# Kernel tuning notes

Measured on AMD Instinct MI355X. Metric: run time of the kernel, lower is better.

Reference implementation:

```python
import jax, jax.numpy as jnp
import numpy as np

H = 16   # num_heads
K = 2    # top_k experts per token


def _layer_norm(x, g, b, eps=1e-5):
    mu = jnp.mean(x, axis=-1, keepdims=True)
    var = jnp.mean(jnp.square(x - mu), axis=-1, keepdims=True)
    return (x - mu) * jax.lax.rsqrt(var + eps) * g + b


def setup_inputs() -> dict:
    key = jax.random.key(0)
    ks = jax.random.split(key, 8)
    B, S, D, E = 2, 2048, 1024, 8
    sc = 0.02
    return {
        "x": jax.random.normal(ks[0], (B, S, D), jnp.float32),
        "wq": jax.random.normal(ks[1], (D, D), jnp.float32) * sc,
        "wk": jax.random.normal(ks[2], (D, D), jnp.float32) * sc,
        "wv": jax.random.normal(ks[3], (D, D), jnp.float32) * sc,
        "wo": jax.random.normal(ks[4], (D, D), jnp.float32) * sc,
        "ln1_g": jnp.ones((D,), jnp.float32),
        "ln1_b": jnp.zeros((D,), jnp.float32),
        "ln2_g": jnp.ones((D,), jnp.float32),
        "ln2_b": jnp.zeros((D,), jnp.float32),
        "router_w": jax.random.normal(ks[5], (E, D), jnp.float32) * sc,
        "expert_w": jax.random.normal(ks[6], (E, D, D), jnp.float32) * sc,
    }


def reference(x, wq, wk, wv, wo, ln1_g, ln1_b, ln2_g, ln2_b, router_w, expert_w):
    B, S, D = x.shape
    E = expert_w.shape[0]
    hd = D // H

    # ---- attention sublayer: x = x + attn(norm1(x)) ----
    h = _layer_norm(x, ln1_g, ln1_b)
    q = (h @ wq.T).reshape(B, S, H, hd).transpose(0, 2, 1, 3)  # bhsd
    k = (h @ wk.T).reshape(B, S, H, hd).transpose(0, 2, 1, 3)
    v = (h @ wv.T).reshape(B, S, H, hd).transpose(0, 2, 1, 3)
    scores = jnp.einsum("bhqd,bhkd->bhqk", q, k) / jnp.sqrt(jnp.float32(hd))
    causal = jnp.tril(jnp.ones((S, S), dtype=bool))
    scores = jnp.where(causal, scores, jnp.finfo(scores.dtype).min)
    probs = jax.nn.softmax(scores, axis=-1)
    attn = jnp.einsum("bhqk,bhkd->bhqd", probs, v)
    attn = attn.transpose(0, 2, 1, 3).reshape(B, S, D) @ wo.T
    x = x + attn

    # ---- MoE sublayer: x = x + moe(norm2(x)) ----
    h2 = _layer_norm(x, ln2_g, ln2_b)
    logits = jnp.einsum("bsd,ed->bse", h2, router_w)          # [B,S,E]
    top_logits, top_ids = jax.lax.top_k(logits, K)            # [B,S,K]
    gates = jax.nn.softmax(top_logits, axis=-1)               # [B,S,K]
    # dense combine weights over experts (E is small): sum_k gate_k * onehot(id_k)
    combine = jnp.sum(jax.nn.one_hot(top_ids, E, dtype=h2.dtype) * gates[..., None], axis=-2)  # [B,S,E]
    # per-token matvec with expert weights: token @ W_e.T for each expert, then weighted sum
    y = jnp.einsum("bsd,eod->bseo", h2, expert_w)             # [B,S,E,D]
    moe_out = jnp.einsum("bse,bseo->bso", combine, y)
    return x + moe_out
```

## Files before the change

kernel.cpp:

```cpp
#include <hip/hip_runtime.h>
#include <hip/hip_bf16.h>
#include <cstdint>


typedef __bf16 bf16;
typedef __bf16 bf16x8 __attribute__((ext_vector_type(8)));
typedef __bf16 bf16x4 __attribute__((ext_vector_type(4)));
typedef float f32x4 __attribute__((ext_vector_type(4)));
typedef float f32x16 __attribute__((ext_vector_type(16)));

#define MFMA(a, b, c) __builtin_amdgcn_mfma_f32_16x16x32_bf16(a, b, c, 0, 0, 0)
#define MFMA32(a, b, c) __builtin_amdgcn_mfma_f32_32x32x16_bf16(a, b, c, 0, 0, 0)

__device__ __forceinline__ void gld16(void* lds, const void* g) {
  __builtin_amdgcn_global_load_lds(
      (const __attribute__((address_space(1))) void*)g,
      (__attribute__((address_space(3))) void*)lds, 16, 0, 0);
}

__device__ __forceinline__ uint32_t pack_hilo(float pv) {
  bf16 h = (bf16)pv;
  bf16 l = (bf16)(pv - (float)h);
  union { bf16 b[2]; uint32_t u; } cv;
  cv.b[0] = h; cv.b[1] = l;
  return cv.u;
}

__global__ void prep_weights(const float* __restrict__ wq, const float* __restrict__ wk,
                             const float* __restrict__ wv, const float* __restrict__ wo,
                             const float* __restrict__ expw,
                             bf16* __restrict__ wqh, bf16* __restrict__ wql,
                             bf16* __restrict__ wkh, bf16* __restrict__ wkl,
                             bf16* __restrict__ wvh, bf16* __restrict__ wvl,
                             bf16* __restrict__ woh, bf16* __restrict__ wol,
                             bf16* __restrict__ ewh) {
  int bid = blockIdx.x;
  if (bid < 4096) {
    int wsel = bid >> 10;
    const float* src = wsel == 0 ? wq : wsel == 1 ? wk : wsel == 2 ? wv : wo;
    bf16* hi = wsel == 0 ? wqh : wsel == 1 ? wkh : wsel == 2 ? wvh : woh;
    bf16* lo = wsel == 0 ? wql : wsel == 1 ? wkl : wsel == 2 ? wvl : wol;
    int i = ((bid & 1023) * 256 + threadIdx.x) * 4;
    float4 v = *(const float4*)(src + i);
    float a[4] = {v.x, v.y, v.z, v.w};
#pragma unroll
    for (int j = 0; j < 4; j++) {
      bf16 h = (bf16)a[j];
      hi[i + j] = h;
      lo[i + j] = (bf16)(a[j] - (float)h);
    }
  } else {
    int i = ((bid - 4096) * 256 + threadIdx.x) * 4;
    float4 v = *(const float4*)(expw + i);
    ewh[i] = (bf16)v.x; ewh[i + 1] = (bf16)v.y;
    ewh[i + 2] = (bf16)v.z; ewh[i + 3] = (bf16)v.w;
  }
}

__global__ void ln_split(const float* __restrict__ x, const float* __restrict__ g,
                         const float* __restrict__ b, bf16* __restrict__ hi,
                         bf16* __restrict__ lo) {
  int tok = blockIdx.x, t = threadIdx.x;
  float4 v = ((const float4*)(x + (size_t)tok * 1024))[t];
  float s = v.x + v.y + v.z + v.w;
  float ss = v.x * v.x + v.y * v.y + v.z * v.z + v.w * v.w;
#pragma unroll
  for (int o = 1; o < 64; o <<= 1) { s += __shfl_xor(s, o); ss += __shfl_xor(ss, o); }
  __shared__ float red[8];
  int w = t >> 6, lane = t & 63;
  if (lane == 0) { red[w] = s; red[4 + w] = ss; }
  __syncthreads();
  s = red[0] + red[1] + red[2] + red[3];
  ss = red[4] + red[5] + red[6] + red[7];
  float mu = s * (1.f / 1024.f);
  float rstd = rsqrtf(ss * (1.f / 1024.f) - mu * mu + 1e-5f);
  float4 gv = ((const float4*)g)[t], bv = ((const float4*)b)[t];
  float y[4] = {(v.x - mu) * rstd * gv.x + bv.x, (v.y - mu) * rstd * gv.y + bv.y,
                (v.z - mu) * rstd * gv.z + bv.z, (v.w - mu) * rstd * gv.w + bv.w};
  size_t o = (size_t)tok * 1024 + t * 4;
#pragma unroll
  for (int j = 0; j < 4; j++) {
    bf16 h = (bf16)y[j];
    hi[o + j] = h;
    lo[o + j] = (bf16)(y[j] - (float)h);
  }
}

__global__ void ln2route(const float* __restrict__ x1, const float* __restrict__ g,
                         const float* __restrict__ b, const float* __restrict__ rw,
                         bf16* __restrict__ h2h, int* __restrict__ eid,
                         float2* __restrict__ gout) {
  int tok = blockIdx.x, t = threadIdx.x;
  float4 v = ((const float4*)(x1 + (size_t)tok * 1024))[t];
  float s = v.x + v.y + v.z + v.w;
  float ss = v.x * v.x + v.y * v.y + v.z * v.z + v.w * v.w;
#pragma unroll
  for (int o = 1; o < 64; o <<= 1) { s += __shfl_xor(s, o); ss += __shfl_xor(ss, o); }
  __shared__ float red[8];
  __shared__ float h2s[1024];
  __shared__ float lg[8];
  int w = t >> 6, lane = t & 63;
  if (lane == 0) { red[w] = s; red[4 + w] = ss; }
  __syncthreads();
  s = red[0] + red[1] + red[2] + red[3];
  ss = red[4] + red[5] + red[6] + red[7];
  float mu = s * (1.f / 1024.f);
  float rstd = rsqrtf(ss * (1.f / 1024.f) - mu * mu + 1e-5f);
  float4 gv = ((const float4*)g)[t], bv = ((const float4*)b)[t];
  float4 y;
  y.x = (v.x - mu) * rstd * gv.x + bv.x;
  y.y = (v.y - mu) * rstd * gv.y + bv.y;
  y.z = (v.z - mu) * rstd * gv.z + bv.z;
  y.w = (v.w - mu) * rstd * gv.w + bv.w;
  ((float4*)h2s)[t] = y;
  size_t o = (size_t)tok * 1024 + t * 4;
  h2h[o] = (bf16)y.x; h2h[o + 1] = (bf16)y.y;
  h2h[o + 2] = (bf16)y.z; h2h[o + 3] = (bf16)y.w;
  __syncthreads();
  float a0 = 0.f, a1 = 0.f;
  const float4* r0 = (const float4*)(rw + (2 * w) * 1024);
  const float4* r1 = (const float4*)(rw + (2 * w + 1) * 1024);
#pragma unroll
  for (int it = 0; it < 4; it++) {
    float4 xv = ((const float4*)h2s)[lane + 64 * it];
    float4 w0 = r0[lane + 64 * it];
    float4 w1 = r1[lane + 64 * it];
    a0 += xv.x * w0.x + xv.y * w0.y + xv.z * w0.z + xv.w * w0.w;
    a1 += xv.x * w1.x + xv.y * w1.y + xv.z * w1.z + xv.w * w1.w;
  }
#pragma unroll
  for (int o2 = 1; o2 < 64; o2 <<= 1) {
    a0 += __shfl_xor(a0, o2);
    a1 += __shfl_xor(a1, o2);
  }
  if (lane == 0) { lg[2 * w] = a0; lg[2 * w + 1] = a1; }
  __syncthreads();
  if (t == 0) {
    int i0 = 0; float l0 = lg[0];
#pragma unroll
    for (int e = 1; e < 8; e++) if (lg[e] > l0) { l0 = lg[e]; i0 = e; }
    int i1 = -1; float l1 = -3e38f;
#pragma unroll
    for (int e = 0; e < 8; e++) if (e != i0 && lg[e] > l1) { l1 = lg[e]; i1 = e; }
    float e1 = __expf(l1 - l0);
    float den = 1.f + e1;
    eid[tok] = i0 | (i1 << 4);
    gout[tok] = make_float2(1.f / den, e1 / den);
  }
}

__global__ void build_lists(const int* __restrict__ eid,
                            const float2* __restrict__ gv,
                            int* __restrict__ tlist, float* __restrict__ glist,
                            int* __restrict__ cnt) {
  int e = blockIdx.x, t = threadIdx.x;
  int lane = t & 63, w = t >> 6;
  __shared__ int wt[4];
  int base = 0;
  for (int c = 0; c < 16; c++) {
    int tok = c * 256 + t;
    int pair = eid[tok];
    int e0 = pair & 15, e1 = pair >> 4;
    bool p = (e0 == e) || (e1 == e);
    float2 g2 = gv[tok];
    float gate = (e0 == e) ? g2.x : g2.y;
    unsigned long long m = __ballot(p);
    int rank = __popcll(m & ((1ull << lane) - 1ull));
    if (lane == 0) wt[w] = __popcll(m);
    __syncthreads();
    int off = base;
    for (int i = 0; i < w; i++) off += wt[i];
    if (p) {
      tlist[e * 4096 + off + rank] = tok;
      glist[e * 4096 + off + rank] = gate;
    }
    base += wt[0] + wt[1] + wt[2] + wt[3];
    __syncthreads();
  }
  if (t == 0) cnt[e] = base;
  int pad = (base + 127) & ~127;
  if (pad > 4096) pad = 4096;
  for (int i = base + t; i < pad; i += 256) {
    tlist[e * 4096 + i] = 0;
    glist[e * 4096 + i] = 0.f;
  }
}

__device__ __forceinline__ void gemm_core_split(
    const bf16* __restrict__ Ah, const bf16* __restrict__ Al,
    const bf16* __restrict__ Bh, const bf16* __restrict__ Bl, int m0, int n0,
    f32x4 (&acc)[4][4]) {
  __shared__ __align__(16) bf16 As_h[4096], As_l[4096], Bs_h[4096], Bs_l[4096];
  int t = threadIdx.x, lane = t & 63, w = t >> 6;
  int i0 = t, i1 = t + 256;
  const bf16* a0h = Ah + (size_t)(m0 + (i0 >> 2)) * 1024 + (i0 & 3) * 8;
  const bf16* a1h = Ah + (size_t)(m0 + (i1 >> 2)) * 1024 + (i1 & 3) * 8;
  const bf16* a0l = Al + (size_t)(m0 + (i0 >> 2)) * 1024 + (i0 & 3) * 8;
  const bf16* a1l = Al + (size_t)(m0 + (i1 >> 2)) * 1024 + (i1 & 3) * 8;
  const bf16* b0h = Bh + (size_t)(n0 + (i0 >> 2)) * 1024 + (i0 & 3) * 8;
  const bf16* b1h = Bh + (size_t)(n0 + (i1 >> 2)) * 1024 + (i1 & 3) * 8;
  const bf16* b0l = Bl + (size_t)(n0 + (i0 >> 2)) * 1024 + (i0 & 3) * 8;
  const bf16* b1l = Bl + (size_t)(n0 + (i1 >> 2)) * 1024 + (i1 & 3) * 8;
  int wm = (w >> 1) * 64, wn = (w & 1) * 64;
  int lr = lane & 15, lq = lane >> 4;
  for (int k0 = 0; k0 < 1024; k0 += 32) {
    __syncthreads();
    gld16(&As_h[i0 * 8], a0h + k0); gld16(&As_h[i1 * 8], a1h + k0);
    gld16(&As_l[i0 * 8], a0l + k0); gld16(&As_l[i1 * 8], a1l + k0);
    gld16(&Bs_h[i0 * 8], b0h + k0); gld16(&Bs_h[i1 * 8], b1h + k0);
    gld16(&Bs_l[i0 * 8], b0l + k0); gld16(&Bs_l[i1 * 8], b1l + k0);
    __syncthreads();
    bf16x8 ah[4], al4[4], bh[4], bl4[4];
#pragma unroll
    for (int i = 0; i < 4; i++) {
      ah[i]  = *(const bf16x8*)&As_h[(wm + i * 16 + lr) * 32 + lq * 8];
      al4[i] = *(const bf16x8*)&As_l[(wm + i * 16 + lr) * 32 + lq * 8];
      bh[i]  = *(const bf16x8*)&Bs_h[(wn + i * 16 + lr) * 32 + lq * 8];
      bl4[i] = *(const bf16x8*)&Bs_l[(wn + i * 16 + lr) * 32 + lq * 8];
    }
#pragma unroll
    for (int i = 0; i < 4; i++)
#pragma unroll
      for (int j = 0; j < 4; j++) {
        f32x4 c = acc[i][j];
        c = MFMA(ah[i], bh[j], c);
        c = MFMA(ah[i], bl4[j], c);
        c = MFMA(al4[i], bh[j], c);
        acc[i][j] = c;
      }
  }
}

__global__ __launch_bounds__(256, 2) void gemm_qkv(
    const bf16* __restrict__ hh, const bf16* __restrict__ hl,
    const bf16* __restrict__ wqh, const bf16* __restrict__ wql,
    const bf16* __restrict__ wkh, const bf16* __restrict__ wkl,
    const bf16* __restrict__ wvh, const bf16* __restrict__ wvl,
    bf16* __restrict__ qh, bf16* __restrict__ ql, bf16* __restrict__ kh,
    bf16* __restrict__ kl, bf16* __restrict__ vth, bf16* __restrict__ vtl) {
  int n0 = blockIdx.x * 128, m0 = blockIdx.y * 128, z = blockIdx.z;
  const bf16 *Bh = wqh, *Bl = wql;
  if (z == 1) { Bh = wkh; Bl = wkl; }
  if (z == 2) { Bh = wvh; Bl = wvl; }
  f32x4 acc[4][4];
#pragma unroll
  for (int i = 0; i < 4; i++)
#pragma unroll
    for (int j = 0; j < 4; j++) acc[i][j] = (f32x4){0.f, 0.f, 0.f, 0.f};
  gemm_core_split(hh, hl, Bh, Bl, m0, n0, acc);
  int t = threadIdx.x, lane = t & 63, w = t >> 6;
  int wm = (w >> 1) * 64, wn = (w & 1) * 64, lr = lane & 15, lq = lane >> 4;
  if (z < 2) {
    bf16* Oh = z == 0 ? qh : kh;
    bf16* Ol = z == 0 ? ql : kl;
    float scale = (z == 0) ? (0.125f * 1.44269504f) : 1.0f;
#pragma unroll
    for (int i = 0; i < 4; i++)
#pragma unroll
      for (int j = 0; j < 4; j++)
#pragma unroll
        for (int r = 0; r < 4; r++) {
          size_t row = m0 + wm + i * 16 + lq * 4 + r;
          int col = n0 + wn + j * 16 + lr;
          float v = acc[i][j][r] * scale;
          bf16 h = (bf16)v;
          Oh[row * 1024 + col] = h;
          Ol[row * 1024 + col] = (bf16)(v - (float)h);
        }
  } else {
    int bb = m0 >> 11;
    int srow0 = m0 & 2047;
#pragma unroll
    for (int i = 0; i < 4; i++)
#pragma unroll
      for (int j = 0; j < 4; j++) {
        int col = n0 + wn + j * 16 + lr;
        int head = col >> 6, d = col & 63;
        int s = srow0 + wm + i * 16 + lq * 4;
        bf16x4 hv, lv;
#pragma unroll
        for (int r = 0; r < 4; r++) {
          float v = acc[i][j][r];
          bf16 h = (bf16)v;
          hv[r] = h;
          lv[r] = (bf16)(v - (float)h);
        }
        size_t off = ((size_t)((bb * 16 + head) * 64 + d)) * 2048 + s;
        *(bf16x4*)(vth + off) = hv;
        *(bf16x4*)(vtl + off) = lv;
      }
  }
}

__global__ __launch_bounds__(256, 2) void gemm_wo(
    const bf16* __restrict__ ah, const bf16* __restrict__ al,
    const bf16* __restrict__ bh, const bf16* __restrict__ bl,
    const float* __restrict__ resid, float* __restrict__ outp) {
  int n0 = blockIdx.x * 128, m0 = blockIdx.y * 128;
  f32x4 acc[4][4];
#pragma unroll
  for (int i = 0; i < 4; i++)
#pragma unroll
    for (int j = 0; j < 4; j++) acc[i][j] = (f32x4){0.f, 0.f, 0.f, 0.f};
  gemm_core_split(ah, al, bh, bl, m0, n0, acc);
  int t = threadIdx.x, lane = t & 63, w = t >> 6;
  int wm = (w >> 1) * 64, wn = (w & 1) * 64, lr = lane & 15, lq = lane >> 4;
#pragma unroll
  for (int i = 0; i < 4; i++)
#pragma unroll
    for (int j = 0; j < 4; j++)
#pragma unroll
      for (int r = 0; r < 4; r++) {
        size_t row = m0 + wm + i * 16 + lq * 4 + r;
        int col = n0 + wn + j * 16 + lr;
        outp[row * 1024 + col] = resid[row * 1024 + col] + acc[i][j][r];
      }
}

__global__ __launch_bounds__(256, 2) void attn_fused(
    const bf16* __restrict__ qh, const bf16* __restrict__ ql,
    const bf16* __restrict__ kh, const bf16* __restrict__ kl,
    const bf16* __restrict__ vth, const bf16* __restrict__ vtl,
    bf16* __restrict__ oh, bf16* __restrict__ ol) {
  const int S = 2048, D = 1024;
  int qt = 15 - blockIdx.y;
  int hb = blockIdx.x;
  int head = hb & 15, b = hb >> 4;
  int qb = qt * 128;
  int t = threadIdx.x, lane = t & 63, w = t >> 6;
  int l31 = lane & 31, l5 = lane >> 5;
  int base = b * S, hcol = head * 64;

  __shared__ __align__(16) bf16 Kh_s[4096], Kl_s[4096];
  __shared__ __align__(16) bf16 Vh_s[4096], Vl_s[4096];
  __shared__ __align__(16) uint32_t Pp[4][32 * 68];

  bf16x8 qfh[4], qfl[4];
  {
    const bf16* p1 = qh + (size_t)(base + qb + w * 32 + l31) * D + hcol + l5 * 8;
    const bf16* p2 = ql + (size_t)(base + qb + w * 32 + l31) * D + hcol + l5 * 8;
#pragma unroll
    for (int c = 0; c < 4; c++) {
      qfh[c] = *(const bf16x8*)(p1 + 16 * c);
      qfl[c] = *(const bf16x8*)(p2 + 16 * c);
    }
  }
  f32x16 O0, O1;
  float lrow[16];
#pragma unroll
  for (int r = 0; r < 16; r++) { O0[r] = 0.f; O1[r] = 0.f; lrow[r] = 0.f; }

  int r0 = t >> 3, p0 = t & 7;
  int r1 = 32 + r0;
  int g0 = p0 ^ (r0 & 7);
  const bf16* k0hp = kh + (size_t)(base + r0) * D + hcol + g0 * 8;
  const bf16* k1hp = kh + (size_t)(base + r1) * D + hcol + g0 * 8;
  const bf16* k0lp = kl + (size_t)(base + r0) * D + hcol + g0 * 8;
  const bf16* k1lp = kl + (size_t)(base + r1) * D + hcol + g0 * 8;
  const bf16* v0hp = vth + (size_t)(hb * 64 + r0) * 2048 + g0 * 8;
  const bf16* v1hp = vth + (size_t)(hb * 64 + r1) * 2048 + g0 * 8;
  const bf16* v0lp = vtl + (size_t)(hb * 64 + r0) * 2048 + g0 * 8;
  const bf16* v1lp = vtl + (size_t)(hb * 64 + r1) * 2048 + g0 * 8;

  int qwmin = qb + w * 32;

  for (int kt = 0; kt <= qb + 64; kt += 64) {
    __syncthreads();
    gld16(&Kh_s[t * 8], k0hp + (size_t)kt * D);
    gld16(&Kh_s[2048 + t * 8], k1hp + (size_t)kt * D);
    gld16(&Kl_s[t * 8], k0lp + (size_t)kt * D);
    gld16(&Kl_s[2048 + t * 8], k1lp + (size_t)kt * D);
    gld16(&Vh_s[t * 8], v0hp + kt);
    gld16(&Vh_s[2048 + t * 8], v1hp + kt);
    gld16(&Vl_s[t * 8], v0lp + kt);
    gld16(&Vl_s[2048 + t * 8], v1lp + kt);
    __syncthreads();
    if (kt > qwmin + 31) continue;
    bool mask0 = (kt + 31 > qwmin);
    bool skip1 = (kt + 32 > qwmin + 31);
    bool mask1 = (kt + 63 > qwmin);
#pragma unroll
    for (int ktile = 0; ktile < 2; ktile++) {
      if (ktile == 1 && skip1) break;
      int keyr = ktile * 32 + l31;
      f32x16 sc;
#pragma unroll
      for (int r = 0; r < 16; r++) sc[r] = 0.f;
#pragma unroll
      for (int c = 0; c < 4; c++) {
        int dg = ((2 * c + l5) ^ (keyr & 7)) * 8;
        bf16x8 kv = *(const bf16x8*)&Kh_s[keyr * 64 + dg];
        bf16x8 km = *(const bf16x8*)&Kl_s[keyr * 64 + dg];
        sc = MFMA32(qfh[c], kv, sc);
        sc = MFMA32(qfl[c], kv, sc);
        sc = MFMA32(qfh[c], km, sc);
      }
      bool m = ktile ? mask1 : mask0;
      int keyg = kt + keyr;
      uint32_t* prow = &Pp[w][ktile * 32 + l31];
#pragma unroll
      for (int r = 0; r < 16; r++) {
        int qlocal = (r & 3) + 8 * (r >> 2) + 4 * l5;
        float sv = sc[r];
        if (m && keyg > qwmin + qlocal) sv = -30000.f;
        float pv = __builtin_amdgcn_exp2f(sv);
        lrow[r] += pv;
        prow[qlocal * 68] = pack_hilo(pv);
      }
    }
#pragma unroll
    for (int c = 0; c < 4; c++) {
      if (skip1 && c >= 2) break;
      const uint32_t* pr = &Pp[w][l31 * 68 + 16 * c + l5 * 8];
      uint32_t pd[8];
      *(uint4*)&pd[0] = *(const uint4*)&pr[0];
      *(uint4*)&pd[4] = *(const uint4*)&pr[4];
      union { uint32_t u[4]; bf16x8 v; } ph_, pl_;
#pragma unroll
      for (int i = 0; i < 4; i++) {
        ph_.u[i] = __builtin_amdgcn_perm(pd[2 * i + 1], pd[2 * i], 0x05040100u);
        pl_.u[i] = __builtin_amdgcn_perm(pd[2 * i + 1], pd[2 * i], 0x07060302u);
      }
#pragma unroll
      for (int dtile = 0; dtile < 2; dtile++) {
        int d = dtile * 32 + l31;
        int kg = ((2 * c + l5) ^ (d & 7)) * 8;
        bf16x8 vb = *(const bf16x8*)&Vh_s[d * 64 + kg];
        bf16x8 vm = *(const bf16x8*)&Vl_s[d * 64 + kg];
        if (dtile == 0) {
          O0 = MFMA32(ph_.v, vb, O0);
          O0 = MFMA32(pl_.v, vb, O0);
          O0 = MFMA32(ph_.v, vm, O0);
        } else {
          O1 = MFMA32(ph_.v, vb, O1);
          O1 = MFMA32(pl_.v, vb, O1);
          O1 = MFMA32(ph_.v, vm, O1);
        }
      }
    }
  }
#pragma unroll
  for (int r = 0; r < 16; r++) {
    float l = lrow[r];
    l += __shfl_xor(l, 1); l += __shfl_xor(l, 2); l += __shfl_xor(l, 4);
    l += __shfl_xor(l, 8); l += __shfl_xor(l, 16);
    float linv = 1.f / l;
    int qlocal = (r & 3) + 8 * (r >> 2) + 4 * l5;
    size_t tok = (size_t)(base + qb + w * 32 + qlocal);
    float v0 = O0[r] * linv;
    float v1 = O1[r] * linv;
    bf16 h0 = (bf16)v0, h1 = (bf16)v1;
    oh[tok * D + hcol + l31] = h0;
    ol[tok * D + hcol + l31] = (bf16)(v0 - (float)h0);
    oh[tok * D + hcol + 32 + l31] = h1;
    ol[tok * D + hcol + 32 + l31] = (bf16)(v1 - (float)h1);
  }
}

__global__ __launch_bounds__(256, 2) void gemm_moe(
    const bf16* __restrict__ A, const bf16* __restrict__ W,
    const int* __restrict__ tlist, const float* __restrict__ glist,
    const int* __restrict__ cnt, float* __restrict__ outp) {
  int e = blockIdx.z;
  int count = cnt[e];
  int m0 = blockIdx.y * 128;
  if (m0 >= count) return;
  int n0 = blockIdx.x * 128;
  const int* tl = tlist + e * 4096;
  const bf16* B = W + (size_t)e * 1024 * 1024;
  __shared__ __align__(16) bf16 As[4096], Bs[4096];
  int t = threadIdx.x, lane = t & 63, w = t >> 6;
  int i0 = t, i1 = t + 256;
  int ra = tl[m0 + (i0 >> 2)], rb = tl[m0 + (i1 >> 2)];
  const bf16* a0 = A + (size_t)ra * 1024 + (i0 & 3) * 8;
  const bf16* a1 = A + (size_t)rb * 1024 + (i1 & 3) * 8;
  const bf16* b0 = B + (size_t)(n0 + (i0 >> 2)) * 1024 + (i0 & 3) * 8;
  const bf16* b1 = B + (size_t)(n0 + (i1 >> 2)) * 1024 + (i1 & 3) * 8;
  int wm = (w >> 1) * 64, wn = (w & 1) * 64, lr = lane & 15, lq = lane >> 4;
  f32x4 acc[4][4];
#pragma unroll
  for (int i = 0; i < 4; i++)
#pragma unroll
    for (int j = 0; j < 4; j++) acc[i][j] = (f32x4){0.f, 0.f, 0.f, 0.f};
  for (int k0 = 0; k0 < 1024; k0 += 32) {
    __syncthreads();
    gld16(&As[i0 * 8], a0 + k0); gld16(&As[i1 * 8], a1 + k0);
    gld16(&Bs[i0 * 8], b0 + k0); gld16(&Bs[i1 * 8], b1 + k0);
    __syncthreads();
    bf16x8 af[4], bfr[4];
#pragma unroll
    for (int i = 0; i < 4; i++) {
      af[i] = *(const bf16x8*)&As[(wm + i * 16 + lr) * 32 + lq * 8];
      bfr[i] = *(const bf16x8*)&Bs[(wn + i * 16 + lr) * 32 + lq * 8];
    }
#pragma unroll
    for (int i = 0; i < 4; i++)
#pragma unroll
      for (int j = 0; j < 4; j++) acc[i][j] = MFMA(af[i], bfr[j], acc[i][j]);
  }
#pragma unroll
  for (int i = 0; i < 4; i++)
#pragma unroll
    for (int r = 0; r < 4; r++) {
      int slot = m0 + wm + i * 16 + lq * 4 + r;
      if (slot < count) {
        int tok = tl[slot];
        float gte = glist[e * 4096 + slot];
#pragma unroll
        for (int j = 0; j < 4; j++) {
          int col = n0 + wn + j * 16 + lr;
          atomicAdd(&outp[(size_t)tok * 1024 + col], gte * acc[i][j][r]);
        }
      }
    }
}

extern "C" void kernel_launch(void* const* d_in, const int* in_sizes, int n_in,
                              void* d_out, int out_size, void* d_ws, size_t ws_size,
                              hipStream_t stream) {
  (void)in_sizes; (void)n_in; (void)out_size; (void)ws_size;
  const float* x    = (const float*)d_in[0];
  const float* wq   = (const float*)d_in[1];
  const float* wk   = (const float*)d_in[2];
  const float* wv   = (const float*)d_in[3];
  const float* wo   = (const float*)d_in[4];
  const float* ln1g = (const float*)d_in[5];
  const float* ln1b = (const float*)d_in[6];
  const float* ln2g = (const float*)d_in[7];
  const float* ln2b = (const float*)d_in[8];
  const float* rw   = (const float*)d_in[9];
  const float* expw = (const float*)d_in[10];
  float* out = (float*)d_out;

  char* p = (char*)d_ws;
  auto take = [&](size_t bytes) -> char* {
    char* r = p;
    p += (bytes + 255) & ~(size_t)255;
    return r;
  };
  const size_t ND2 = 4096ull * 1024 * 2;
  const size_t WD2 = 1024ull * 1024 * 2;
  bf16* h_hi = (bf16*)take(ND2); bf16* h_lo = (bf16*)take(ND2);
  bf16* wqh = (bf16*)take(WD2); bf16* wql = (bf16*)take(WD2);
  bf16* wkh = (bf16*)take(WD2); bf16* wkl = (bf16*)take(WD2);
  bf16* wvh = (bf16*)take(WD2); bf16* wvl = (bf16*)take(WD2);
  bf16* woh = (bf16*)take(WD2); bf16* wol = (bf16*)take(WD2);
  bf16* q_hi = (bf16*)take(ND2); bf16* q_lo = (bf16*)take(ND2);
  bf16* k_hi = (bf16*)take(ND2); bf16* k_lo = (bf16*)take(ND2);
  bf16* vt_hi = (bf16*)take(ND2); bf16* vt_lo = (bf16*)take(ND2);
  bf16* a_hi = (bf16*)take(ND2); bf16* a_lo = (bf16*)take(ND2);
  bf16* h2h  = (bf16*)take(ND2);
  bf16* ewh  = (bf16*)take(8ull * 1024 * 1024 * 2);
  int*   tlist  = (int*)take(8ull * 4096 * 4);
  float* glist  = (float*)take(8ull * 4096 * 4);
  int*   cnt    = (int*)take(64);
  int*   reid   = (int*)take(4096 * 4);
  float2* rg    = (float2*)take(4096 * 8);

  prep_weights<<<12288, 256, 0, stream>>>(wq, wk, wv, wo, expw, wqh, wql, wkh,
                                          wkl, wvh, wvl, woh, wol, ewh);
  ln_split<<<4096, 256, 0, stream>>>(x, ln1g, ln1b, h_hi, h_lo);
  gemm_qkv<<<dim3(8, 32, 3), 256, 0, stream>>>(h_hi, h_lo, wqh, wql, wkh, wkl,
                                               wvh, wvl, q_hi, q_lo, k_hi, k_lo,
                                               vt_hi, vt_lo);
  attn_fused<<<dim3(32, 16), 256, 0, stream>>>(q_hi, q_lo, k_hi, k_lo, vt_hi,
                                               vt_lo, a_hi, a_lo);
  gemm_wo<<<dim3(8, 32), 256, 0, stream>>>(a_hi, a_lo, woh, wol, x, out);
  ln2route<<<4096, 256, 0, stream>>>(out, ln2g, ln2b, rw, h2h, reid, rg);
  build_lists<<<8, 256, 0, stream>>>(reid, rg, tlist, glist, cnt);
  gemm_moe<<<dim3(8, 32, 8), 256, 0, stream>>>(h2h, ewh, tlist, glist, cnt,
                                               out);
}
```

Baseline: 414.6 us.

## Double-buffer attention K/V tiles in 32-key chunks and raise occupancy bounds

The attention kernel now streams K/V in 32-key chunks with two LDS buffers, prefetching the next chunk while computing the current one, and drops one of the two barriers per iteration. The V tile uses a new swizzle and the P scratch shrinks, which lowers LDS use. Q-tile scheduling is reordered so long and short causal tiles alternate. Launch bounds rise to 3 blocks per CU for attention and 4 for the GEMMs, which may force register spilling.

Result: slower. 442.2 us (+6.7%).

```diff
diff --git a/kernel.cpp b/kernel.cpp
--- a/kernel.cpp
+++ b/kernel.cpp
@@ -231,7 +231,7 @@
   }
 }
 
-__global__ __launch_bounds__(256, 2) void gemm_qkv(
+__global__ __launch_bounds__(256, 4) void gemm_qkv(
     const bf16* __restrict__ hh, const bf16* __restrict__ hl,
     const bf16* __restrict__ wqh, const bf16* __restrict__ wql,
     const bf16* __restrict__ wkh, const bf16* __restrict__ wkl,
@@ -292,7 +292,7 @@
   }
 }
 
-__global__ __launch_bounds__(256, 2) void gemm_wo(
+__global__ __launch_bounds__(256, 4) void gemm_wo(
     const bf16* __restrict__ ah, const bf16* __restrict__ al,
     const bf16* __restrict__ bh, const bf16* __restrict__ bl,
     const float* __restrict__ resid, float* __restrict__ outp) {
@@ -317,13 +317,14 @@
       }
 }
 
-__global__ __launch_bounds__(256, 2) void attn_fused(
+__global__ __launch_bounds__(256, 3) void attn_fused(
     const bf16* __restrict__ qh, const bf16* __restrict__ ql,
     const bf16* __restrict__ kh, const bf16* __restrict__ kl,
     const bf16* __restrict__ vth, const bf16* __restrict__ vtl,
     bf16* __restrict__ oh, bf16* __restrict__ ol) {
   const int S = 2048, D = 1024;
-  int qt = 15 - blockIdx.y;
+  int y = blockIdx.y;
+  int qt = (y < 8) ? (15 - y) : (y - 8);
   int hb = blockIdx.x;
   int head = hb & 15, b = hb >> 4;
   int qb = qt * 128;
@@ -331,9 +332,9 @@
   int l31 = lane & 31, l5 = lane >> 5;
   int base = b * S, hcol = head * 64;
 
-  __shared__ __align__(16) bf16 Kh_s[4096], Kl_s[4096];
-  __shared__ __align__(16) bf16 Vh_s[4096], Vl_s[4096];
-  __shared__ __align__(16) uint32_t Pp[4][32 * 68];
+  __shared__ __align__(16) bf16 Kh_s[2][2048], Kl_s[2][2048];
+  __shared__ __align__(16) bf16 Vh_s[2][2048], Vl_s[2][2048];
+  __shared__ __align__(16) uint32_t Pp[4][32 * 36];
 
   bf16x8 qfh[4], qfl[4];
   {
@@ -350,94 +351,92 @@
 #pragma unroll
   for (int r = 0; r < 16; r++) { O0[r] = 0.f; O1[r] = 0.f; lrow[r] = 0.f; }
 
-  int r0 = t >> 3, p0 = t & 7;
-  int r1 = 32 + r0;
-  int g0 = p0 ^ (r0 & 7);
-  const bf16* k0hp = kh + (size_t)(base + r0) * D + hcol + g0 * 8;
-  const bf16* k1hp = kh + (size_t)(base + r1) * D + hcol + g0 * 8;
-  const bf16* k0lp = kl + (size_t)(base + r0) * D + hcol + g0 * 8;
-  const bf16* k1lp = kl + (size_t)(base + r1) * D + hcol + g0 * 8;
-  const bf16* v0hp = vth + (size_t)(hb * 64 + r0) * 2048 + g0 * 8;
-  const bf16* v1hp = vth + (size_t)(hb * 64 + r1) * 2048 + g0 * 8;
-  const bf16* v0lp = vtl + (size_t)(hb * 64 + r0) * 2048 + g0 * 8;
-  const bf16* v1lp = vtl + (size_t)(hb * 64 + r1) * 2048 + g0 * 8;
+  int krow = t >> 3;
+  int kg = (t & 7) ^ (krow & 7);
+  const bf16* kph = kh + (size_t)(base + krow) * D + hcol + kg * 8;
+  const bf16* kpl = kl + (size_t)(base + krow) * D + hcol + kg * 8;
+  int vd = ((t >> 3) << 1) | ((t >> 2) & 1);
+  int vg = ((t & 3) - (t >> 3)) & 3;
+  const bf16* vph = vth + (size_t)(hb * 64 + vd) * 2048 + vg * 8;
+  const bf16* vpl = vtl + (size_t)(hb * 64 + vd) * 2048 + vg * 8;
 
   int qwmin = qb + w * 32;
-
-  for (int kt = 0; kt <= qb + 64; kt += 64) {
-    __syncthreads();
-    gld16(&Kh_s[t * 8], k0hp + (size_t)kt * D);
-    gld16(&Kh_s[2048 + t * 8], k1hp + (size_t)kt * D);
-    gld16(&Kl_s[t * 8], k0lp + (size_t)kt * D);
-    gld16(&Kl_s[2048 + t * 8], k1lp + (size_t)kt * D);
-    gld16(&Vh_s[t * 8], v0hp + kt);
-    gld16(&Vh_s[2048 + t * 8], v1hp + kt);
-    gld16(&Vl_s[t * 8], v0lp + kt);
-    gld16(&Vl_s[2048 + t * 8], v1lp + kt);
-    __syncthreads();
-    if (kt > qwmin + 31) continue;
-    bool mask0 = (kt + 31 > qwmin);
-    bool skip1 = (kt + 32 > qwmin + 31);
-    bool mask1 = (kt + 63 > qwmin);
-#pragma unroll
-    for (int ktile = 0; ktile < 2; ktile++) {
-      if (ktile == 1 && skip1) break;
-      int keyr = ktile * 32 + l31;
+  int nch = (qb + 128) >> 5;
+
+  gld16(&Kh_s[0][t * 8], kph);
+  gld16(&Kl_s[0][t * 8], kpl);
+  gld16(&Vh_s[0][t * 8], vph);
+  gld16(&Vl_s[0][t * 8], vpl);
+  __syncthreads();
+
+  for (int it = 0; it < nch; it++) {
+    int ib = it & 1;
+    if (it + 1 < nch) {
+      int jb = ib ^ 1;
+      size_t ko = (size_t)(it + 1) * 32 * D;
+      int vo = (it + 1) * 32;
+      gld16(&Kh_s[jb][t * 8], kph + ko);
+      gld16(&Kl_s[jb][t * 8], kpl + ko);
+      gld16(&Vh_s[jb][t * 8], vph + vo);
+      gld16(&Vl_s[jb][t * 8], vpl + vo);
+    }
+    int kt = it << 5;
+    if (kt <= qwmin + 31) {
+      bool need_mask = (kt + 31 > qwmin);
       f32x16 sc;
 #pragma unroll
       for (int r = 0; r < 16; r++) sc[r] = 0.f;
 #pragma unroll
       for (int c = 0; c < 4; c++) {
-        int dg = ((2 * c + l5) ^ (keyr & 7)) * 8;
-        bf16x8 kv = *(const bf16x8*)&Kh_s[keyr * 64 + dg];
-        bf16x8 km = *(const bf16x8*)&Kl_s[keyr * 64 + dg];
+        int pg = ((2 * c + l5) ^ (l31 & 7)) * 8;
+        bf16x8 kv = *(const bf16x8*)&Kh_s[ib][l31 * 64 + pg];
+        bf16x8 km = *(const bf16x8*)&Kl_s[ib][l31 * 64 + pg];
         sc = MFMA32(qfh[c], kv, sc);
         sc = MFMA32(qfl[c], kv, sc);
         sc = MFMA32(qfh[c], km, sc);
       }
-      bool m = ktile ? mask1 : mask0;
-      int keyg = kt + keyr;
-      uint32_t* prow = &Pp[w][ktile * 32 + l31];
+      uint32_t* prow = &Pp[w][l31];
 #pragma unroll
       for (int r = 0; r < 16; r++) {
         int qlocal = (r & 3) + 8 * (r >> 2) + 4 * l5;
         float sv = sc[r];
-        if (m && keyg > qwmin + qlocal) sv = -30000.f;
+        if (need_mask && kt + l31 > qwmin + qlocal) sv = -30000.f;
         float pv = __builtin_amdgcn_exp2f(sv);
         lrow[r] += pv;
-        prow[qlocal * 68] = pack_hilo(pv);
-      }
-    }
-#pragma unroll
-    for (int c = 0; c < 4; c++) {
-      if (skip1 && c >= 2) break;
-      const uint32_t* pr = &Pp[w][l31 * 68 + 16 * c + l5 * 8];
-      uint32_t pd[8];
-      *(uint4*)&pd[0] = *(const uint4*)&pr[0];
-      *(uint4*)&pd[4] = *(const uint4*)&pr[4];
-      union { uint32_t u[4]; bf16x8 v; } ph_, pl_;
-#pragma unroll
-      for (int i = 0; i < 4; i++) {
-        ph_.u[i] = __builtin_amdgcn_perm(pd[2 * i + 1], pd[2 * i], 0x05040100u);
-        pl_.u[i] = __builtin_amdgcn_perm(pd[2 * i + 1], pd[2 * i], 0x07060302u);
-      }
-#pragma unroll
-      for (int dtile = 0; dtile < 2; dtile++) {
-        int d = dtile * 32 + l31;
-        int kg = ((2 * c + l5) ^ (d & 7)) * 8;
-        bf16x8 vb = *(const bf16x8*)&Vh_s[d * 64 + kg];
-        bf16x8 vm = *(const bf16x8*)&Vl_s[d * 64 + kg];
-        if (dtile == 0) {
-          O0 = MFMA32(ph_.v, vb, O0);
-          O0 = MFMA32(pl_.v, vb, O0);
-          O0 = MFMA32(ph_.v, vm, O0);
-        } else {
-          O1 = MFMA32(ph_.v, vb, O1);
-          O1 = MFMA32(pl_.v, vb, O1);
-          O1 = MFMA32(ph_.v, vm, O1);
+        prow[qlocal * 36] = pack_hilo(pv);
+      }
+#pragma unroll
+      for (int kc = 0; kc < 2; kc++) {
+        const uint32_t* pr = &Pp[w][l31 * 36 + kc * 16 + l5 * 8];
+        uint32_t pd[8];
+        *(uint4*)&pd[0] = *(const uint4*)&pr[0];
+        *(uint4*)&pd[4] = *(const uint4*)&pr[4];
+        union { uint32_t u[4]; bf16x8 v; } ph_, pl_;
+#pragma unroll
+        for (int i = 0; i < 4; i++) {
+          ph_.u[i] = __builtin_amdgcn_perm(pd[2 * i + 1], pd[2 * i], 0x05040100u);
+          pl_.u[i] = __builtin_amdgcn_perm(pd[2 * i + 1], pd[2 * i], 0x07060302u);
         }
-      }
-    }
+        int g = 2 * kc + l5;
+#pragma unroll
+        for (int dtile = 0; dtile < 2; dtile++) {
+          int d = dtile * 32 + l31;
+          int slot = ((d >> 1) << 3) | ((d & 1) << 2) | ((g + (d >> 1)) & 3);
+          bf16x8 vb = *(const bf16x8*)&Vh_s[ib][slot * 8];
+          bf16x8 vm = *(const bf16x8*)&Vl_s[ib][slot * 8];
+          if (dtile == 0) {
+            O0 = MFMA32(ph_.v, vb, O0);
+            O0 = MFMA32(pl_.v, vb, O0);
+            O0 = MFMA32(ph_.v, vm, O0);
+          } else {
+            O1 = MFMA32(ph_.v, vb, O1);
+            O1 = MFMA32(pl_.v, vb, O1);
+            O1 = MFMA32(ph_.v, vm, O1);
+          }
+        }
+      }
+    }
+    __syncthreads();
   }
 #pragma unroll
   for (int r = 0; r < 16; r++) {
@@ -457,7 +456,7 @@
   }
 }
 
-__global__ __launch_bounds__(256, 2) void gemm_moe(
+__global__ __launch_bounds__(256, 4) void gemm_moe(
     const bf16* __restrict__ A, const bf16* __restrict__ W,
     const int* __restrict__ tlist, const float* __restrict__ glist,
     const int* __restrict__ cnt, float* __restrict__ outp) {
```
